# Kernel optimization log

Measured on AMD Instinct MI355X. Metric: run time of the kernel, lower is better.

The kernel has to match this reference:

```python
import jax, jax.numpy as jnp
import numpy as np

NUM_NODES = 10000
NUM_EDGES = 160000
NUM_REL = 4
IN_DIM = 15
HID = 512
NUM_GRAPHS = 64


def setup_inputs() -> dict:
    key = jax.random.key(0)
    ks = jax.random.split(key, 8)
    x = jax.random.normal(ks[0], (NUM_NODES, IN_DIM), dtype=jnp.float32)
    edge_index = jax.random.randint(ks[1], (2, NUM_EDGES), 0, NUM_NODES, dtype=jnp.int64)
    edge_type = jax.random.randint(ks[2], (NUM_EDGES,), 0, NUM_REL, dtype=jnp.int64)
    batch = jnp.sort(jax.random.randint(ks[3], (NUM_NODES,), 0, NUM_GRAPHS, dtype=jnp.int64))
    # glorot-style scaled params
    W1_rel = jax.random.normal(ks[4], (NUM_REL, IN_DIM, HID), dtype=jnp.float32) * (1.0 / np.sqrt(IN_DIM))
    W1_root = jax.random.normal(ks[5], (IN_DIM, HID), dtype=jnp.float32) * (1.0 / np.sqrt(IN_DIM))
    b1 = jnp.zeros((HID,), dtype=jnp.float32)
    W2_rel = jax.random.normal(ks[6], (NUM_REL, HID, HID), dtype=jnp.float32) * (1.0 / np.sqrt(HID))
    W2_root = jax.random.normal(ks[7], (HID, HID), dtype=jnp.float32) * (1.0 / np.sqrt(HID))
    b2 = jnp.zeros((HID,), dtype=jnp.float32)
    return {"x": x, "edge_index": edge_index, "edge_type": edge_type, "batch": batch,
            "W1_rel": W1_rel, "W1_root": W1_root, "b1": b1,
            "W2_rel": W2_rel, "W2_root": W2_root, "b2": b2}


def _rgcn_conv(x, src, tgt, seg, W_rel, W_root, b):
    """PyG RGCNConv (non-decomposed, aggr='mean'):
    out[i] = x[i]@W_root + b + sum_r (mean_{j in N_r(i)} x[j]) @ W_r.
    seg = tgt*NUM_REL + edge_type combines (target, relation) into one segment id
    so a single segment_sum handles the per-relation mean."""
    E = src.shape[0]
    msgs = x[src]                                              # [E, d_in] irregular gather
    sums = jax.ops.segment_sum(msgs, seg, num_segments=x.shape[0] * NUM_REL)
    cnts = jax.ops.segment_sum(jnp.ones((E,), x.dtype), seg, num_segments=x.shape[0] * NUM_REL)
    mean = sums / jnp.maximum(cnts, 1.0)[:, None]              # [N*R, d_in]
    mean = mean.reshape(x.shape[0], NUM_REL, x.shape[1])       # [N, R, d_in]
    return jnp.einsum('nrd,rdo->no', mean, W_rel) + x @ W_root + b


def reference(x, edge_index, edge_type, batch, W1_rel, W1_root, b1, W2_rel, W2_root, b2):
    src, tgt = edge_index[0], edge_index[1]
    seg = tgt * NUM_REL + edge_type
    h = jax.nn.relu(_rgcn_conv(x, src, tgt, seg, W1_rel, W1_root, b1))
    h = jax.nn.relu(_rgcn_conv(h, src, tgt, seg, W2_rel, W2_root, b2))
    # global_mean_pool over graphs
    gsum = jax.ops.segment_sum(h, batch, num_segments=NUM_GRAPHS)
    gcnt = jax.ops.segment_sum(jnp.ones((h.shape[0],), h.dtype), batch, num_segments=NUM_GRAPHS)
    return gsum / jnp.maximum(gcnt, 1.0)[:, None]              # [NUM_GRAPHS, HID]
```

## Files before the change

### kernel.cpp

```cpp
#include <hip/hip_runtime.h>

#define N_NODES 10000
#define N_EDGES 160000
#define N_REL 4
#define IN_DIM 15
#define HID 512
#define N_GRAPHS 64
#define NSEG (N_NODES * N_REL)
#define K2 (N_REL * HID + HID)
#define MAXC 64

typedef __attribute__((ext_vector_type(8))) short s16x8;
typedef __attribute__((ext_vector_type(4))) short s16x4;
typedef __attribute__((ext_vector_type(4))) float f32x4;

__device__ __forceinline__ float bf2f(short s) {
    return __uint_as_float(((unsigned)(unsigned short)s) << 16);
}
__device__ __forceinline__ short f2bf(float f) {
    unsigned u = __float_as_uint(f);
    u += 0x7fff + ((u >> 16) & 1);
    return (short)(u >> 16);
}

#define B_CNT    0u
#define B_ELIST  160000u
#define B_GINV   10400000u
#define B_W1B    10400256u
#define B_H      10478080u
#define B_MEAN2  20718080u
#define B_BT     61678080u

__global__ void bin_kernel(const int* __restrict__ src, const int* __restrict__ tgt,
                           const int* __restrict__ et, const int* __restrict__ batch,
                           const float* __restrict__ W1_rel, const float* __restrict__ W1_root,
                           int* __restrict__ cnt, int* __restrict__ elist,
                           float* __restrict__ out, float* __restrict__ ginv,
                           short* __restrict__ W1b) {
    int e = blockIdx.x * blockDim.x + threadIdx.x;
    if (e < N_GRAPHS * HID) out[e] = 0.f;
    if (e < N_GRAPHS) {
        int g = e;
        int s, en;
        { int l = 0, hsz = N_NODES;
          while (l < hsz) { int m = (l + hsz) >> 1; if (batch[m] < g) l = m + 1; else hsz = m; }
          s = l; }
        { int l = s, hsz = N_NODES;
          while (l < hsz) { int m = (l + hsz) >> 1; if (batch[m] < g + 1) l = m + 1; else hsz = m; }
          en = l; }
        ginv[g] = (en > s) ? 1.0f / (float)(en - s) : 0.f;
    }
    if (e < 19 * 512) {
        int gidx = e >> 9, o = e & 511;
        short w[4];
        #pragma unroll
        for (int j = 0; j < 4; ++j) {
            int k = gidx * 4 + j;
            float v;
            if (k < 60)      v = W1_rel[(long)k * HID + o];
            else if (k < 75) v = W1_root[(long)(k - 60) * HID + o];
            else             v = 0.f;
            w[j] = f2bf(v);
        }
        *(s16x4*)(W1b + (long)e * 4) = *(s16x4*)w;
    }
    if (e >= N_EDGES) return;
    int seg = tgt[e] * N_REL + et[e];
    int pos = atomicAdd(&cnt[seg], 1);
    if (pos < MAXC) elist[seg * MAXC + pos] = src[e];
}

#define NPB 16
__global__ __launch_bounds__(512) void layer1_kernel(
        const float* __restrict__ x, const int* __restrict__ cnts,
        const int* __restrict__ elist, const short* __restrict__ W1b,
        const float* __restrict__ b1, short* __restrict__ h) {
    const int nb = blockIdx.x * NPB;
    __shared__ float f[NPB][76];
    const int t = threadIdx.x;
    for (int task = t; task < NPB * 60; task += 512) {
        int m = task / 60, k = task - m * 60;
        int n = nb + m;
        int seg = n * N_REL + k / IN_DIM;
        int d = k % IN_DIM;
        int cnt = cnts[seg]; if (cnt > MAXC) cnt = MAXC;
        int b = seg * MAXC;
        float acc = 0.f;
        for (int i = 0; i < cnt; ++i) acc += x[elist[b + i] * IN_DIM + d];
        f[m][k] = (cnt > 0) ? acc / (float)cnt : 0.f;
    }
    for (int task = t; task < NPB * 16; task += 512) {
        int m = task >> 4, d = task & 15;
        f[m][60 + d] = (d < IN_DIM) ? x[(nb + m) * IN_DIM + d] : 0.f;
    }
    __syncthreads();
    const int o = t;
    float acc[NPB];
    const float bias = b1[o];
    #pragma unroll
    for (int m = 0; m < NPB; ++m) acc[m] = bias;
    #pragma unroll 2
    for (int k4 = 0; k4 < 76; k4 += 4) {
        s16x4 wv = *(const s16x4*)(W1b + (long)((k4 >> 2) * 512 + o) * 4);
        float w0 = bf2f(wv[0]), w1 = bf2f(wv[1]), w2 = bf2f(wv[2]), w3 = bf2f(wv[3]);
        #pragma unroll
        for (int m = 0; m < NPB; ++m) {
            float4 fv = *(const float4*)&f[m][k4];
            acc[m] = fmaf(fv.x, w0, fmaf(fv.y, w1, fmaf(fv.z, w2, fmaf(fv.w, w3, acc[m]))));
        }
    }
    #pragma unroll
    for (int m = 0; m < NPB; ++m)
        h[(long)(nb + m) * HID + o] = f2bf(fmaxf(acc[m], 0.0f));
}

#define MEAN2_BLOCKS (NSEG / 4)
__global__ __launch_bounds__(256) void mean2_wtrans_kernel(
        const short* __restrict__ h, const int* __restrict__ cnts,
        const int* __restrict__ elist, short* __restrict__ mean2,
        const float* __restrict__ W2_rel, const float* __restrict__ W2_root,
        short* __restrict__ Bt) {
    __shared__ float tile[64][65];
    if (blockIdx.x < MEAN2_BLOCKS) {
        const int wid = (blockIdx.x << 2) + (threadIdx.x >> 6);
        const int lane = threadIdx.x & 63;
        int cnt = cnts[wid]; if (cnt > MAXC) cnt = MAXC;
        const int b = wid * MAXC;
        float acc[8] = {0.f,0.f,0.f,0.f,0.f,0.f,0.f,0.f};
        int el = 0;
        if (lane < cnt) el = elist[b + lane];
        for (int i = 0; i < cnt; ++i) {
            int row = __shfl(el, i, 64);
            const s16x8 v = *(const s16x8*)(h + (long)row * HID + lane * 8);
            #pragma unroll
            for (int j = 0; j < 8; ++j) acc[j] += bf2f(v[j]);
        }
        const float inv = (cnt > 0) ? 1.0f / (float)cnt : 0.0f;
        s16x8 o;
        #pragma unroll
        for (int j = 0; j < 8; ++j) o[j] = f2bf(acc[j] * inv);
        *(s16x8*)(mean2 + (long)wid * HID + lane * 8) = o;
    } else {
        const int bx = blockIdx.x - MEAN2_BLOCKS;
        const int k0 = (bx % 40) * 64;
        const int o0 = (bx / 40) * 64;
        const int t = threadIdx.x;
        #pragma unroll
        for (int i = 0; i < 16; ++i) {
            int idx = t + i * 256;
            int kk = idx >> 6, oo = idx & 63;
            int k = k0 + kk;
            float v = (k < N_REL * HID) ? W2_rel[(long)k * HID + o0 + oo]
                                        : W2_root[(long)(k - N_REL * HID) * HID + o0 + oo];
            tile[kk][oo] = v;
        }
        __syncthreads();
        #pragma unroll
        for (int i = 0; i < 16; ++i) {
            int idx = t + i * 256;
            int oo = idx >> 6, kk = idx & 63;
            Bt[(long)(o0 + oo) * K2 + k0 + kk] = f2bf(tile[kk][oo]);
        }
    }
}

#define GM 64
#define GN 128
#define GK 64
#define NT (K2 / GK)
#define NWG (4 * ((N_NODES + GM - 1) / GM))
__global__ __launch_bounds__(256) void gemm2_kernel(
        const short* __restrict__ mean2, const short* __restrict__ h,
        const short* __restrict__ Bt, const float* __restrict__ b2,
        const int* __restrict__ batch, const float* __restrict__ ginv,
        float* __restrict__ out) {
    __shared__ __align__(16) short Al[2][GM * GK];
    __shared__ __align__(16) short Bl[2][GN * GK];
    const int tid = threadIdx.x;
    const int lane = tid & 63;
    const int w = tid >> 6;
    const int orig = blockIdx.x;
    const int q = NWG >> 3, r = NWG & 7;
    const int xcd = orig & 7, cidx = orig >> 3;
    const int wgid = (xcd < r ? xcd * (q + 1) : r * (q + 1) + (xcd - r) * q) + cidx;
    const int m0 = (wgid >> 2) * GM;
    const int n0 = (wgid & 3) * GN;
    const int l15 = lane & 15, lg = lane >> 4;

    f32x4 acc[4][2];
    #pragma unroll
    for (int a = 0; a < 4; ++a)
        #pragma unroll
        for (int bb = 0; bb < 2; ++bb)
            acc[a][bb] = (f32x4){0.f, 0.f, 0.f, 0.f};

#define STAGE(buf, k0)                                                           \
    {                                                                            \
        _Pragma("unroll")                                                        \
        for (int i = 0; i < 2; ++i) {                                            \
            int c = tid + i * 256;                                               \
            int row = c >> 3, slot = c & 7;                                      \
            int srcslot = slot ^ (row & 7);                                      \
            int n = m0 + row; if (n > N_NODES - 1) n = N_NODES - 1;              \
            int kg = (k0) + srcslot * 8;                                         \
            const short* gsrc = (kg < N_REL * HID)                               \
                ? (mean2 + (long)n * (N_REL * HID) + kg)                         \
                : (h + (long)n * HID + (kg - N_REL * HID));                      \
            __builtin_amdgcn_global_load_lds(                                    \
                (const __attribute__((address_space(1))) void*)gsrc,             \
                (__attribute__((address_space(3))) void*)(Al[buf] + c * 8),      \
                16, 0, 0);                                                       \
        }                                                                        \
        _Pragma("unroll")                                                        \
        for (int i = 0; i < 4; ++i) {                                            \
            int c = tid + i * 256;                                               \
            int row = c >> 3, slot = c & 7;                                      \
            int srcslot = slot ^ (row & 7);                                      \
            const short* gsrc = Bt + (long)(n0 + row) * K2 + (k0) + srcslot * 8; \
            __builtin_amdgcn_global_load_lds(                                    \
                (const __attribute__((address_space(1))) void*)gsrc,             \
                (__attribute__((address_space(3))) void*)(Bl[buf] + c * 8),      \
                16, 0, 0);                                                       \
        }                                                                        \
    }

    STAGE(0, 0);
    asm volatile("s_waitcnt vmcnt(0)" ::: "memory");
    __builtin_amdgcn_s_barrier();
    asm volatile("" ::: "memory");

    int cur = 0;
    #pragma unroll 1
    for (int t = 0; t < NT; ++t) {
        if (t + 1 < NT) STAGE(cur ^ 1, (t + 1) * GK);
        #pragma unroll
        for (int hh = 0; hh < 2; ++hh) {
            s16x8 af[4], bfr[2];
            #pragma unroll
            for (int fm = 0; fm < 4; ++fm) {
                int row = fm * 16 + l15;
                int slot = (hh * 4 + lg) ^ (row & 7);
                af[fm] = *(const s16x8*)(Al[cur] + row * GK + slot * 8);
            }
            #pragma unroll
            for (int fn = 0; fn < 2; ++fn) {
                int row = w * 32 + fn * 16 + l15;
                int slot = (hh * 4 + lg) ^ (row & 7);
                bfr[fn] = *(const s16x8*)(Bl[cur] + row * GK + slot * 8);
            }
            #pragma unroll
            for (int fm = 0; fm < 4; ++fm)
                #pragma unroll
                for (int fn = 0; fn < 2; ++fn)
                    asm("v_mfma_f32_16x16x32_bf16 %0, %1, %2, %0"
                        : "+v"(acc[fm][fn]) : "v"(af[fm]), "v"(bfr[fn]));
        }
        asm volatile("s_waitcnt vmcnt(0)" ::: "memory");
        __builtin_amdgcn_s_barrier();
        asm volatile("" ::: "memory");
        cur ^= 1;
    }
#undef STAGE

    const int col0 = n0 + w * 32 + l15;
    const float bias0 = b2[col0];
    const float bias1 = b2[col0 + 16];
    int cur_g = -1;
    float s0 = 0.f, s1 = 0.f;
    #pragma unroll
    for (int fm = 0; fm < 4; ++fm) {
        #pragma unroll
        for (int r2 = 0; r2 < 4; ++r2) {
            int n = m0 + fm * 16 + 4 * lg + r2;
            if (n < N_NODES) {
                int g = batch[n];
                if (g != cur_g) {
                    if (cur_g >= 0) {
                        float gi = ginv[cur_g];
                        float* og = out + (long)cur_g * HID;
                        atomicAdd(og + col0,      s0 * gi);
                        atomicAdd(og + col0 + 16, s1 * gi);
                    }
                    cur_g = g; s0 = 0.f; s1 = 0.f;
                }
                s0 += fmaxf(acc[fm][0][r2] + bias0, 0.f);
                s1 += fmaxf(acc[fm][1][r2] + bias1, 0.f);
            }
        }
    }
    if (cur_g >= 0) {
        float gi = ginv[cur_g];
        float* og = out + (long)cur_g * HID;
        atomicAdd(og + col0,      s0 * gi);
        atomicAdd(og + col0 + 16, s1 * gi);
    }
}

extern "C" void kernel_launch(void* const* d_in, const int* in_sizes, int n_in,
                              void* d_out, int out_size, void* d_ws, size_t ws_size,
                              hipStream_t stream) {
    const float* x       = (const float*)d_in[0];
    const int*   ei      = (const int*)d_in[1];
    const int*   src     = ei;
    const int*   tgt     = ei + N_EDGES;
    const int*   etype   = (const int*)d_in[2];
    const int*   batch   = (const int*)d_in[3];
    const float* W1_rel  = (const float*)d_in[4];
    const float* W1_root = (const float*)d_in[5];
    const float* b1      = (const float*)d_in[6];
    const float* W2_rel  = (const float*)d_in[7];
    const float* W2_root = (const float*)d_in[8];
    const float* b2      = (const float*)d_in[9];
    float* out = (float*)d_out;

    char* ws = (char*)d_ws;
    int*   cnts  = (int*)(ws + B_CNT);
    int*   elist = (int*)(ws + B_ELIST);
    float* ginv  = (float*)(ws + B_GINV);
    short* W1b   = (short*)(ws + B_W1B);
    short* h     = (short*)(ws + B_H);
    short* mean2 = (short*)(ws + B_MEAN2);
    short* Bt    = (short*)(ws + B_BT);

    hipMemsetAsync(cnts, 0, NSEG * sizeof(int), stream);

    bin_kernel<<<(N_EDGES + 255) / 256, 256, 0, stream>>>(
        src, tgt, etype, batch, W1_rel, W1_root, cnts, elist, out, ginv, W1b);

    layer1_kernel<<<N_NODES / NPB, 512, 0, stream>>>(x, cnts, elist, W1b, b1, h);

    mean2_wtrans_kernel<<<MEAN2_BLOCKS + (K2 / 64) * (HID / 64), 256, 0, stream>>>(
        h, cnts, elist, mean2, W2_rel, W2_root, Bt);

    gemm2_kernel<<<NWG, 256, 0, stream>>>(mean2, h, Bt, b2, batch, ginv, out);
}
```

Before: 125.0 us.

## Fuse memset, binning, layer1 and mean2 into one cooperative persistent kernel

Replaces the memset plus three separate kernel launches with a single cooperative kernel of 512 persistent blocks that uses grid-wide syncs between phases: zeroing and weight prep, edge binning, layer-1 compute, then mean2 aggregation and W2 transpose. The aim is to cut launch overhead and inter-kernel gaps. In exchange, grid.sync barriers are added, parallelism is capped at 512 blocks of 256 threads, and layer-1 now handles two output columns per thread, which raises register pressure and halves its threads per block.

```diff
diff --git a/kernel.cpp b/kernel.cpp
--- a/kernel.cpp
+++ b/kernel.cpp
@@ -1,4 +1,6 @@
 #include <hip/hip_runtime.h>
+#include <hip/hip_cooperative_groups.h>
+namespace cg = cooperative_groups;
 
 #define N_NODES 10000
 #define N_EDGES 160000
@@ -10,6 +12,10 @@
 #define K2 (N_REL * HID + HID)
 #define MAXC 64
 
+#define PRE_BLOCKS 512
+#define PRE_THREADS 256
+#define PRE_GT (PRE_BLOCKS * PRE_THREADS)
+
 typedef __attribute__((ext_vector_type(8))) short s16x8;
 typedef __attribute__((ext_vector_type(4))) short s16x4;
 typedef __attribute__((ext_vector_type(4))) float f32x4;
@@ -31,16 +37,34 @@
 #define B_MEAN2  20718080u
 #define B_BT     61678080u
 
-__global__ void bin_kernel(const int* __restrict__ src, const int* __restrict__ tgt,
-                           const int* __restrict__ et, const int* __restrict__ batch,
-                           const float* __restrict__ W1_rel, const float* __restrict__ W1_root,
-                           int* __restrict__ cnt, int* __restrict__ elist,
-                           float* __restrict__ out, float* __restrict__ ginv,
-                           short* __restrict__ W1b) {
-    int e = blockIdx.x * blockDim.x + threadIdx.x;
-    if (e < N_GRAPHS * HID) out[e] = 0.f;
-    if (e < N_GRAPHS) {
-        int g = e;
+#define NPB 16
+#define L1_JOBS (N_NODES / NPB)
+#define MEAN2_JOBS (NSEG / 4)
+#define WT_JOBS ((K2 / 64) * (HID / 64))
+
+__global__ __launch_bounds__(PRE_THREADS) void pre_kernel(
+        const float* __restrict__ x, const int* __restrict__ src,
+        const int* __restrict__ tgt, const int* __restrict__ et,
+        const int* __restrict__ batch,
+        const float* __restrict__ W1_rel, const float* __restrict__ W1_root,
+        const float* __restrict__ b1,
+        const float* __restrict__ W2_rel, const float* __restrict__ W2_root,
+        int* __restrict__ cnts, int* __restrict__ elist,
+        float* __restrict__ ginv, short* __restrict__ W1b,
+        short* __restrict__ h, short* __restrict__ mean2,
+        short* __restrict__ Bt, float* __restrict__ out) {
+    cg::grid_group grid = cg::this_grid();
+    const int t = threadIdx.x;
+    const int bid = blockIdx.x;
+    const int gid = bid * PRE_THREADS + t;
+
+    __shared__ float f[NPB][76];
+    __shared__ float tile[64][65];
+
+    if (gid < NSEG) cnts[gid] = 0;
+    if (gid < N_GRAPHS * HID) out[gid] = 0.f;
+    if (gid < N_GRAPHS) {
+        int g = gid;
         int s, en;
         { int l = 0, hsz = N_NODES;
           while (l < hsz) { int m = (l + hsz) >> 1; if (batch[m] < g) l = m + 1; else hsz = m; }
@@ -50,8 +74,8 @@
           en = l; }
         ginv[g] = (en > s) ? 1.0f / (float)(en - s) : 0.f;
     }
-    if (e < 19 * 512) {
-        int gidx = e >> 9, o = e & 511;
+    if (gid < 19 * 512) {
+        int gidx = gid >> 9, o = gid & 511;
         short w[4];
         #pragma unroll
         for (int j = 0; j < 4; ++j) {
@@ -62,104 +86,103 @@
             else             v = 0.f;
             w[j] = f2bf(v);
         }
-        *(s16x4*)(W1b + (long)e * 4) = *(s16x4*)w;
-    }
-    if (e >= N_EDGES) return;
-    int seg = tgt[e] * N_REL + et[e];
-    int pos = atomicAdd(&cnt[seg], 1);
-    if (pos < MAXC) elist[seg * MAXC + pos] = src[e];
-}
-
-#define NPB 16
-__global__ __launch_bounds__(512) void layer1_kernel(
-        const float* __restrict__ x, const int* __restrict__ cnts,
-        const int* __restrict__ elist, const short* __restrict__ W1b,
-        const float* __restrict__ b1, short* __restrict__ h) {
-    const int nb = blockIdx.x * NPB;
-    __shared__ float f[NPB][76];
-    const int t = threadIdx.x;
-    for (int task = t; task < NPB * 60; task += 512) {
-        int m = task / 60, k = task - m * 60;
-        int n = nb + m;
-        int seg = n * N_REL + k / IN_DIM;
-        int d = k % IN_DIM;
-        int cnt = cnts[seg]; if (cnt > MAXC) cnt = MAXC;
-        int b = seg * MAXC;
-        float acc = 0.f;
-        for (int i = 0; i < cnt; ++i) acc += x[elist[b + i] * IN_DIM + d];
-        f[m][k] = (cnt > 0) ? acc / (float)cnt : 0.f;
-    }
-    for (int task = t; task < NPB * 16; task += 512) {
-        int m = task >> 4, d = task & 15;
-        f[m][60 + d] = (d < IN_DIM) ? x[(nb + m) * IN_DIM + d] : 0.f;
-    }
-    __syncthreads();
-    const int o = t;
-    float acc[NPB];
-    const float bias = b1[o];
-    #pragma unroll
-    for (int m = 0; m < NPB; ++m) acc[m] = bias;
-    #pragma unroll 2
-    for (int k4 = 0; k4 < 76; k4 += 4) {
-        s16x4 wv = *(const s16x4*)(W1b + (long)((k4 >> 2) * 512 + o) * 4);
-        float w0 = bf2f(wv[0]), w1 = bf2f(wv[1]), w2 = bf2f(wv[2]), w3 = bf2f(wv[3]);
+        *(s16x4*)(W1b + (long)gid * 4) = *(s16x4*)w;
+    }
+    grid.sync();
+
+    for (int e = gid; e < N_EDGES; e += PRE_GT) {
+        int seg = tgt[e] * N_REL + et[e];
+        int pos = atomicAdd(&cnts[seg], 1);
+        if (pos < MAXC) elist[seg * MAXC + pos] = src[e];
+    }
+    grid.sync();
+
+    for (int jb = bid; jb < L1_JOBS; jb += PRE_BLOCKS) {
+        const int nb = jb * NPB;
+        for (int task = t; task < NPB * 60; task += PRE_THREADS) {
+            int m = task / 60, k = task - m * 60;
+            int n = nb + m;
+            int seg = n * N_REL + k / IN_DIM;
+            int d = k % IN_DIM;
+            int cnt = cnts[seg]; if (cnt > MAXC) cnt = MAXC;
+            int b = seg * MAXC;
+            float acc = 0.f;
+            for (int i = 0; i < cnt; ++i) acc += x[elist[b + i] * IN_DIM + d];
+            f[m][k] = (cnt > 0) ? acc / (float)cnt : 0.f;
+        }
+        for (int task = t; task < NPB * 16; task += PRE_THREADS) {
+            int m = task >> 4, d = task & 15;
+            f[m][60 + d] = (d < IN_DIM) ? x[(nb + m) * IN_DIM + d] : 0.f;
+        }
+        __syncthreads();
+        const int o0 = t, o1 = t + 256;
+        float acc0[NPB], acc1[NPB];
+        const float bias0 = b1[o0], bias1 = b1[o1];
+        #pragma unroll
+        for (int m = 0; m < NPB; ++m) { acc0[m] = bias0; acc1[m] = bias1; }
+        #pragma unroll 2
+        for (int k4 = 0; k4 < 76; k4 += 4) {
+            s16x4 wv0 = *(const s16x4*)(W1b + (long)((k4 >> 2) * 512 + o0) * 4);
+            s16x4 wv1 = *(const s16x4*)(W1b + (long)((k4 >> 2) * 512 + o1) * 4);
+            float a0 = bf2f(wv0[0]), a1 = bf2f(wv0[1]), a2 = bf2f(wv0[2]), a3 = bf2f(wv0[3]);
+            float c0 = bf2f(wv1[0]), c1 = bf2f(wv1[1]), c2 = bf2f(wv1[2]), c3 = bf2f(wv1[3]);
+            #pragma unroll
+            for (int m = 0; m < NPB; ++m) {
+                float4 fv = *(const float4*)&f[m][k4];
+                acc0[m] = fmaf(fv.x, a0, fmaf(fv.y, a1, fmaf(fv.z, a2, fmaf(fv.w, a3, acc0[m]))));
+                acc1[m] = fmaf(fv.x, c0, fmaf(fv.y, c1, fmaf(fv.z, c2, fmaf(fv.w, c3, acc1[m]))));
+            }
+        }
         #pragma unroll
         for (int m = 0; m < NPB; ++m) {
-            float4 fv = *(const float4*)&f[m][k4];
-            acc[m] = fmaf(fv.x, w0, fmaf(fv.y, w1, fmaf(fv.z, w2, fmaf(fv.w, w3, acc[m]))));
-        }
-    }
-    #pragma unroll
-    for (int m = 0; m < NPB; ++m)
-        h[(long)(nb + m) * HID + o] = f2bf(fmaxf(acc[m], 0.0f));
-}
-
-#define MEAN2_BLOCKS (NSEG / 4)
-__global__ __launch_bounds__(256) void mean2_wtrans_kernel(
-        const short* __restrict__ h, const int* __restrict__ cnts,
-        const int* __restrict__ elist, short* __restrict__ mean2,
-        const float* __restrict__ W2_rel, const float* __restrict__ W2_root,
-        short* __restrict__ Bt) {
-    __shared__ float tile[64][65];
-    if (blockIdx.x < MEAN2_BLOCKS) {
-        const int wid = (blockIdx.x << 2) + (threadIdx.x >> 6);
-        const int lane = threadIdx.x & 63;
-        int cnt = cnts[wid]; if (cnt > MAXC) cnt = MAXC;
-        const int b = wid * MAXC;
-        float acc[8] = {0.f,0.f,0.f,0.f,0.f,0.f,0.f,0.f};
-        int el = 0;
-        if (lane < cnt) el = elist[b + lane];
-        for (int i = 0; i < cnt; ++i) {
-            int row = __shfl(el, i, 64);
-            const s16x8 v = *(const s16x8*)(h + (long)row * HID + lane * 8);
-            #pragma unroll
-            for (int j = 0; j < 8; ++j) acc[j] += bf2f(v[j]);
-        }
-        const float inv = (cnt > 0) ? 1.0f / (float)cnt : 0.0f;
-        s16x8 o;
-        #pragma unroll
-        for (int j = 0; j < 8; ++j) o[j] = f2bf(acc[j] * inv);
-        *(s16x8*)(mean2 + (long)wid * HID + lane * 8) = o;
-    } else {
-        const int bx = blockIdx.x - MEAN2_BLOCKS;
-        const int k0 = (bx % 40) * 64;
-        const int o0 = (bx / 40) * 64;
-        const int t = threadIdx.x;
-        #pragma unroll
-        for (int i = 0; i < 16; ++i) {
-            int idx = t + i * 256;
-            int kk = idx >> 6, oo = idx & 63;
-            int k = k0 + kk;
-            float v = (k < N_REL * HID) ? W2_rel[(long)k * HID + o0 + oo]
-                                        : W2_root[(long)(k - N_REL * HID) * HID + o0 + oo];
-            tile[kk][oo] = v;
+            h[(long)(nb + m) * HID + o0] = f2bf(fmaxf(acc0[m], 0.0f));
+            h[(long)(nb + m) * HID + o1] = f2bf(fmaxf(acc1[m], 0.0f));
         }
         __syncthreads();
-        #pragma unroll
-        for (int i = 0; i < 16; ++i) {
-            int idx = t + i * 256;
-            int oo = idx >> 6, kk = idx & 63;
-            Bt[(long)(o0 + oo) * K2 + k0 + kk] = f2bf(tile[kk][oo]);
+    }
+    grid.sync();
+
+    for (int j = bid; j < MEAN2_JOBS + WT_JOBS; j += PRE_BLOCKS) {
+        if (j < MEAN2_JOBS) {
+            const int wid = (j << 2) + (t >> 6);
+            const int lane = t & 63;
+            int cnt = cnts[wid]; if (cnt > MAXC) cnt = MAXC;
+            const int b = wid * MAXC;
+            float acc[8] = {0.f,0.f,0.f,0.f,0.f,0.f,0.f,0.f};
+            int el = 0;
+            if (lane < cnt) el = elist[b + lane];
+            for (int i = 0; i < cnt; ++i) {
+                int row = __shfl(el, i, 64);
+                const s16x8 v = *(const s16x8*)(h + (long)row * HID + lane * 8);
+                #pragma unroll
+                for (int jj = 0; jj < 8; ++jj) acc[jj] += bf2f(v[jj]);
+            }
+            const float inv = (cnt > 0) ? 1.0f / (float)cnt : 0.0f;
+            s16x8 o;
+            #pragma unroll
+            for (int jj = 0; jj < 8; ++jj) o[jj] = f2bf(acc[jj] * inv);
+            *(s16x8*)(mean2 + (long)wid * HID + lane * 8) = o;
+        } else {
+            const int bx = j - MEAN2_JOBS;
+            const int k0 = (bx % 40) * 64;
+            const int o0 = (bx / 40) * 64;
+            #pragma unroll
+            for (int i = 0; i < 16; ++i) {
+                int idx = t + i * 256;
+                int kk = idx >> 6, oo = idx & 63;
+                int k = k0 + kk;
+                float v = (k < N_REL * HID) ? W2_rel[(long)k * HID + o0 + oo]
+                                            : W2_root[(long)(k - N_REL * HID) * HID + o0 + oo];
+                tile[kk][oo] = v;
+            }
+            __syncthreads();
+            #pragma unroll
+            for (int i = 0; i < 16; ++i) {
+                int idx = t + i * 256;
+                int oo = idx >> 6, kk = idx & 63;
+                Bt[(long)(o0 + oo) * K2 + k0 + kk] = f2bf(tile[kk][oo]);
+            }
+            __syncthreads();
         }
     }
 }
@@ -322,15 +345,14 @@
     short* mean2 = (short*)(ws + B_MEAN2);
     short* Bt    = (short*)(ws + B_BT);
 
-    hipMemsetAsync(cnts, 0, NSEG * sizeof(int), stream);
-
-    bin_kernel<<<(N_EDGES + 255) / 256, 256, 0, stream>>>(
-        src, tgt, etype, batch, W1_rel, W1_root, cnts, elist, out, ginv, W1b);
-
-    layer1_kernel<<<N_NODES / NPB, 512, 0, stream>>>(x, cnts, elist, W1b, b1, h);
-
-    mean2_wtrans_kernel<<<MEAN2_BLOCKS + (K2 / 64) * (HID / 64), 256, 0, stream>>>(
-        h, cnts, elist, mean2, W2_rel, W2_root, Bt);
+    void* kargs[] = {
+        (void*)&x, (void*)&src, (void*)&tgt, (void*)&etype, (void*)&batch,
+        (void*)&W1_rel, (void*)&W1_root, (void*)&b1, (void*)&W2_rel, (void*)&W2_root,
+        (void*)&cnts, (void*)&elist, (void*)&ginv, (void*)&W1b,
+        (void*)&h, (void*)&mean2, (void*)&Bt, (void*)&out
+    };
+    hipLaunchCooperativeKernel((void*)pre_kernel, dim3(PRE_BLOCKS), dim3(PRE_THREADS),
+                               kargs, 0, stream);
 
     gemm2_kernel<<<NWG, 256, 0, stream>>>(mean2, h, Bt, b2, batch, ginv, out);
 }
```

Measured after the change: 325.2 us. 160% more time.
